# Kernel tuning notes

Measured on AMD Instinct MI355X. Metric: run time of the kernel, lower is better.

## Reference

```python
import jax, jax.numpy as jnp
import numpy as np

N = 50000
C = 128
E = 800000
STEPS = 3


def setup_inputs() -> dict:
    key = jax.random.key(0)
    ks = jax.random.split(key, 8)
    x = jax.random.normal(ks[0], (N, C), dtype=jnp.float32)
    edge_index = jax.random.randint(ks[1], (2, E), 0, N, dtype=jnp.int64)
    s = 1.0 / np.sqrt(C)
    W_lin = jax.random.uniform(ks[2], (C, C), jnp.float32, -s, s)   # nn.Linear(C, C, bias=False)
    W_ih = jax.random.uniform(ks[3], (3 * C, C), jnp.float32, -s, s)  # GRUCell weight_ih
    W_hh = jax.random.uniform(ks[4], (3 * C, C), jnp.float32, -s, s)  # GRUCell weight_hh
    b_ih = jax.random.uniform(ks[5], (3 * C,), jnp.float32, -s, s)
    b_hh = jax.random.uniform(ks[6], (3 * C,), jnp.float32, -s, s)
    return {"x": x, "edge_index": edge_index, "W_lin": W_lin,
            "W_ih": W_ih, "W_hh": W_hh, "b_ih": b_ih, "b_hh": b_hh}


def _gru_cell(inp, h, W_ih, W_hh, b_ih, b_hh):
    # torch.nn.GRUCell math
    gi = inp @ W_ih.T + b_ih   # [N, 3C]
    gh = h @ W_hh.T + b_hh     # [N, 3C]
    i_r, i_z, i_n = jnp.split(gi, 3, axis=-1)
    h_r, h_z, h_n = jnp.split(gh, 3, axis=-1)
    r = jax.nn.sigmoid(i_r + h_r)
    z = jax.nn.sigmoid(i_z + h_z)
    n = jnp.tanh(i_n + r * h_n)
    return (1.0 - z) * n + z * h


def reference(x, edge_index, W_lin, W_ih, W_hh, b_ih, b_hh):
    src = edge_index[0]
    dst = edge_index[1]
    state = x
    for _ in range(STEPS):
        m = state @ W_lin.T                       # [N, C] dense transform
        msgs = jnp.take(m, src, axis=0)           # [E, C] gather
        propagated = jax.ops.segment_sum(msgs, dst, num_segments=N)  # scatter-add
        state = _gru_cell(propagated, state, W_ih, W_hh, b_ih, b_hh)
    return state
```

## Files before the change

### kernel.cpp

```cpp
#include <hip/hip_runtime.h>

#define NN 50000
#define CC 128
#define EE 800000
#define NT 1563
#define NBLK 196

typedef short bf16x8 __attribute__((ext_vector_type(8)));
typedef float f32x4 __attribute__((ext_vector_type(4)));

__device__ __forceinline__ float bf2f(unsigned int u16) {
  union { unsigned int u; float f; } x; x.u = u16 << 16; return x.f;
}
__device__ __forceinline__ unsigned short f2bf(float f) {
  union { float f; unsigned int u; } x; x.f = f;
  unsigned int u = x.u;
  unsigned int r = (u + 0x7fffu + ((u >> 16) & 1u)) >> 16;
  return (unsigned short)r;
}
__device__ __forceinline__ float fsigmoid(float x) {
  return __fdividef(1.f, 1.f + __expf(-x));
}
__device__ __forceinline__ float ftanh(float x) {
  return 1.f - __fdividef(2.f, 1.f + __expf(2.f * x));
}

__global__ void cast_f2b_k(const float* __restrict__ in, unsigned short* __restrict__ out, int n4) {
  int i = blockIdx.x * blockDim.x + threadIdx.x;
  int stride = gridDim.x * blockDim.x;
  for (; i < n4; i += stride) {
    float4 v = ((const float4*)in)[i];
    ushort4 o;
    o.x = f2bf(v.x); o.y = f2bf(v.y); o.z = f2bf(v.z); o.w = f2bf(v.w);
    ((ushort4*)out)[i] = o;
  }
}

__global__ __launch_bounds__(256) void wprep_k(const float* __restrict__ Wih,
                                               const float* __restrict__ Wlin,
                                               const float* __restrict__ Whh,
                                               unsigned short* __restrict__ Wcb,
                                               unsigned short* __restrict__ Whhb) {
  if (blockIdx.x < 192) {
    int gid = blockIdx.x * 256 + threadIdx.x;
    int i = gid >> 7, j = gid & 127;
    float acc = 0.f;
    #pragma unroll 8
    for (int k = 0; k < 128; ++k)
      acc += Wih[i * 128 + k] * Wlin[k * 128 + j];
    Wcb[i * 128 + j] = f2bf(acc);
  } else {
    int i = (blockIdx.x - 192) * 256 + threadIdx.x;
    float4 v = ((const float4*)Whh)[i];
    ushort4 o;
    o.x = f2bf(v.x); o.y = f2bf(v.y); o.z = f2bf(v.z); o.w = f2bf(v.w);
    ((ushort4*)Whhb)[i] = o;
  }
}

__global__ void zero_k(int* __restrict__ p, int n) {
  int i = blockIdx.x * blockDim.x + threadIdx.x;
  if (i < n) p[i] = 0;
}

__global__ void hist_k(const int* __restrict__ dst, int* __restrict__ cntrep,
                       int* __restrict__ rank, int n) {
  int i = blockIdx.x * blockDim.x + threadIdx.x;
  int rep = blockIdx.x & 7;
  if (i < n) rank[i] = atomicAdd(&cntrep[rep * NN + dst[i]], 1);
}

__global__ __launch_bounds__(256) void scan1_k(int* __restrict__ cntrep,
                                               int* __restrict__ rowptr,
                                               int* __restrict__ bsum, int N) {
  __shared__ int wtot[4];
  int tid = threadIdx.x, lane = tid & 63, w = tid >> 6;
  int i = blockIdx.x * 256 + tid;
  int v = 0;
  if (i < N) {
    int s = 0;
    #pragma unroll
    for (int r = 0; r < 8; ++r) {
      int c = cntrep[r * NN + i];
      cntrep[r * NN + i] = s;
      s += c;
    }
    v = s;
  }
  int x = v;
  #pragma unroll
  for (int off = 1; off < 64; off <<= 1) {
    int t = __shfl_up(x, off, 64);
    if (lane >= off) x += t;
  }
  if (lane == 63) wtot[w] = x;
  __syncthreads();
  int woff = 0;
  for (int j = 0; j < w; ++j) woff += wtot[j];
  int excl = x - v + woff;
  if (i < N) rowptr[i] = excl;
  if (tid == 255) bsum[blockIdx.x] = excl + v;
}

__global__ __launch_bounds__(256) void scan2_k(int* __restrict__ bsum, int* __restrict__ rowptr, int NB) {
  __shared__ int wtot[4];
  int tid = threadIdx.x, lane = tid & 63, w = tid >> 6;
  int v = (tid < NB) ? bsum[tid] : 0;
  int x = v;
  #pragma unroll
  for (int off = 1; off < 64; off <<= 1) {
    int t = __shfl_up(x, off, 64);
    if (lane >= off) x += t;
  }
  if (lane == 63) wtot[w] = x;
  __syncthreads();
  int woff = 0;
  for (int j = 0; j < w; ++j) woff += wtot[j];
  int excl = x - v + woff;
  if (tid < NB) bsum[tid] = excl;
  if (tid == 255) rowptr[NN] = excl + v;
}

__global__ void scan3_k(int* __restrict__ rowptr, const int* __restrict__ bsum, int N) {
  int i = blockIdx.x * 256 + threadIdx.x;
  if (i < N) rowptr[i] = rowptr[i] + bsum[i >> 8];
}

__global__ void fill_k(const int* __restrict__ src, const int* __restrict__ dst,
                       const int* __restrict__ rank, const int* __restrict__ rowptr,
                       const int* __restrict__ cntrep, int* __restrict__ colx, int n4) {
  int i = blockIdx.x * blockDim.x + threadIdx.x;
  if (i < n4) {
    int4 s = ((const int4*)src)[i];
    int4 d = ((const int4*)dst)[i];
    int4 r = ((const int4*)rank)[i];
    int base = ((i >> 6) & 7) * NN;
    colx[rowptr[d.x] + cntrep[base + d.x] + r.x] = s.x;
    colx[rowptr[d.y] + cntrep[base + d.y] + r.y] = s.y;
    colx[rowptr[d.z] + cntrep[base + d.z] + r.z] = s.z;
    colx[rowptr[d.w] + cntrep[base + d.w] + r.w] = s.w;
  }
}

__global__ __launch_bounds__(256) void agg3_k(const unsigned short* __restrict__ M,
                                              const int* __restrict__ rowptr,
                                              const int* __restrict__ colx,
                                              unsigned short* __restrict__ P, int N) {
  int wid = (blockIdx.x * 256 + threadIdx.x) >> 6;
  int lane = threadIdx.x & 63;
  if (wid >= N) return;
  int beg = rowptr[wid], end = rowptr[wid + 1];
  int slot = lane >> 4, li = lane & 15;
  float a0 = 0.f, a1 = 0.f, a2 = 0.f, a3 = 0.f, a4 = 0.f, a5 = 0.f, a6 = 0.f, a7 = 0.f;
  #define ACC(v) do { \
    a0 += bf2f((v).x & 0xffffu); a1 += bf2f((v).x >> 16); \
    a2 += bf2f((v).y & 0xffffu); a3 += bf2f((v).y >> 16); \
    a4 += bf2f((v).z & 0xffffu); a5 += bf2f((v).z >> 16); \
    a6 += bf2f((v).w & 0xffffu); a7 += bf2f((v).w >> 16); } while (0)
  int n = end - beg;
  int i = 0;
  for (; i + 16 <= n; i += 16) {
    int e = beg + i + slot;
    int s0 = colx[e], s1 = colx[e + 4], s2 = colx[e + 8], s3 = colx[e + 12];
    uint4 v0 = *(const uint4*)(M + s0 * CC + li * 8);
    uint4 v1 = *(const uint4*)(M + s1 * CC + li * 8);
    uint4 v2 = *(const uint4*)(M + s2 * CC + li * 8);
    uint4 v3 = *(const uint4*)(M + s3 * CC + li * 8);
    ACC(v0); ACC(v1); ACC(v2); ACC(v3);
  }
  for (; i + 4 <= n; i += 4) {
    int e = beg + i + slot;
    int s = colx[e];
    uint4 v = *(const uint4*)(M + s * CC + li * 8);
    ACC(v);
  }
  int rem = n - i;
  if (slot < rem) {
    int e = beg + i + slot;
    int s = colx[e];
    uint4 v = *(const uint4*)(M + s * CC + li * 8);
    ACC(v);
  }
  #undef ACC
  #pragma unroll
  for (int m = 16; m <= 32; m <<= 1) {
    a0 += __shfl_xor(a0, m, 64); a1 += __shfl_xor(a1, m, 64);
    a2 += __shfl_xor(a2, m, 64); a3 += __shfl_xor(a3, m, 64);
    a4 += __shfl_xor(a4, m, 64); a5 += __shfl_xor(a5, m, 64);
    a6 += __shfl_xor(a6, m, 64); a7 += __shfl_xor(a7, m, 64);
  }
  if (slot == 0) {
    uint4 o;
    o.x = (unsigned int)f2bf(a0) | ((unsigned int)f2bf(a1) << 16);
    o.y = (unsigned int)f2bf(a2) | ((unsigned int)f2bf(a3) << 16);
    o.z = (unsigned int)f2bf(a4) | ((unsigned int)f2bf(a5) << 16);
    o.w = (unsigned int)f2bf(a6) | ((unsigned int)f2bf(a7) << 16);
    *(uint4*)(P + wid * CC + li * 8) = o;
  }
}

__global__ __launch_bounds__(512, 2) void gru4_k(const unsigned short* __restrict__ Pb,
                                                 const unsigned short* __restrict__ Sb_in,
                                                 unsigned short* __restrict__ Sb_out,
                                                 float* __restrict__ fout,
                                                 const unsigned short* __restrict__ Wcb,
                                                 const unsigned short* __restrict__ Whhb,
                                                 const float* __restrict__ bih,
                                                 const float* __restrict__ bhh) {
  __shared__ unsigned short sA[2][2][32][128];
  const int tid = threadIdx.x;
  const int lane = tid & 63, w = tid >> 6;
  const int l15 = lane & 15, l4 = lane >> 4;

  const int cg = w * 16 + l15;

  bf16x8 Breg[6][4];
  #pragma unroll
  for (int pi = 0; pi < 6; ++pi) {
    const unsigned short* Wm = (pi < 3) ? Wcb : Whhb;
    int p = (pi < 3) ? pi : pi - 3;
    const unsigned short* base = Wm + (p * 128 + cg) * 128 + l4 * 8;
    #pragma unroll
    for (int ks = 0; ks < 4; ++ks)
      Breg[pi][ks] = *(const bf16x8*)(base + ks * 32);
  }

  const float bir = bih[cg], biz = bih[cg + 128], bin_ = bih[cg + 256];
  const float bhr = bhh[cg], bhz = bhh[cg + 128], bhn = bhh[cg + 256];

  auto loadA = [&](int t, uint4* r) {
    int rowbase = t * 32;
    #pragma unroll
    for (int k = 0; k < 2; ++k) {
      int idx = k * 512 + tid;
      int mat = idx >> 9, j = idx & 511, row = j >> 4, ch = j & 15;
      int grow = rowbase + row;
      const unsigned short* srcp = mat ? Sb_in : Pb;
      r[k] = (grow < NN) ? *(const uint4*)(srcp + grow * 128 + ch * 8) : make_uint4(0, 0, 0, 0);
    }
  };
  auto writeA = [&](int buf, const uint4* r) {
    #pragma unroll
    for (int k = 0; k < 2; ++k) {
      int idx = k * 512 + tid;
      int mat = idx >> 9, j = idx & 511, row = j >> 4, ch = j & 15;
      *(uint4*)&sA[buf][mat][row][((ch ^ (row & 15)) * 8)] = r[k];
    }
  };

  uint4 pre[2];
  int t0 = blockIdx.x;
  loadA(t0, pre);
  writeA(0, pre);
  int cur = 0;
  for (int t = t0; t < NT; t += 256) {
    __syncthreads();
    int tn = t + 256;
    uint4 nxt[2];
    if (tn < NT) loadA(tn, nxt);

    f32x4 acc[6][2] = {};
    #pragma unroll
    for (int ks = 0; ks < 4; ++ks) {
      bf16x8 a[2][2];
      #pragma unroll
      for (int mat = 0; mat < 2; ++mat)
        #pragma unroll
        for (int rt = 0; rt < 2; ++rt) {
          int row = rt * 16 + l15;
          a[mat][rt] = *(const bf16x8*)&sA[cur][mat][row][(((ks * 4 + l4) ^ l15) * 8)];
        }
      #pragma unroll
      for (int pi = 0; pi < 6; ++pi) {
        int am = (pi < 3) ? 0 : 1;
        acc[pi][0] = __builtin_amdgcn_mfma_f32_16x16x32_bf16(a[am][0], Breg[pi][ks], acc[pi][0], 0, 0, 0);
        acc[pi][1] = __builtin_amdgcn_mfma_f32_16x16x32_bf16(a[am][1], Breg[pi][ks], acc[pi][1], 0, 0, 0);
      }
    }

    int rowbase = t * 32;
    #pragma unroll
    for (int rt = 0; rt < 2; ++rt)
      #pragma unroll
      for (int i = 0; i < 4; ++i) {
        int row_loc = rt * 16 + l4 * 4 + i;
        int row = rowbase + row_loc;
        if (row < NN) {
          float gir = acc[0][rt][i] + bir;
          float giz = acc[1][rt][i] + biz;
          float gin = acc[2][rt][i] + bin_;
          float ghr = acc[3][rt][i] + bhr;
          float ghz = acc[4][rt][i] + bhz;
          float ghn = acc[5][rt][i] + bhn;
          float r = fsigmoid(gir + ghr);
          float z = fsigmoid(giz + ghz);
          float n = ftanh(gin + r * ghn);
          float h = bf2f((unsigned int)sA[cur][1][row_loc][(((cg >> 3) ^ (row_loc & 15)) << 3) + (cg & 7)]);
          float o = n + z * (h - n);
          if (fout) fout[row * 128 + cg] = o;
          else      Sb_out[row * 128 + cg] = f2bf(o);
        }
      }
    if (tn < NT) writeA(cur ^ 1, nxt);
    cur ^= 1;
  }
}

extern "C" void kernel_launch(void* const* d_in, const int* in_sizes, int n_in,
                              void* d_out, int out_size, void* d_ws, size_t ws_size,
                              hipStream_t stream) {
  const float* x    = (const float*)d_in[0];
  const int*   ei   = (const int*)d_in[1];
  const float* Wlin = (const float*)d_in[2];
  const float* Wih  = (const float*)d_in[3];
  const float* Whh  = (const float*)d_in[4];
  const float* bih  = (const float*)d_in[5];
  const float* bhh  = (const float*)d_in[6];
  float* out = (float*)d_out;

  char* ws = (char*)d_ws;
  size_t off = 0;
  auto alloc = [&](size_t bytes) -> void* {
    void* p = ws + off;
    off += (bytes + 255) & ~(size_t)255;
    return p;
  };
  unsigned short* SbA  = (unsigned short*)alloc((size_t)NN * CC * 2);
  unsigned short* SbB  = (unsigned short*)alloc((size_t)NN * CC * 2);
  unsigned short* Prb  = (unsigned short*)alloc((size_t)NN * CC * 2);
  unsigned short* Wcb  = (unsigned short*)alloc((size_t)3 * CC * CC * 2);
  unsigned short* Whhb = (unsigned short*)alloc((size_t)3 * CC * CC * 2);
  int* rowptr = (int*)alloc((size_t)(NN + 1) * 4);
  int* cntrep = (int*)alloc((size_t)8 * NN * 4);
  int* rank   = (int*)alloc((size_t)EE * 4);
  int* colx   = (int*)alloc((size_t)EE * 4);
  int* bsum   = (int*)alloc(256 * 4);

  const int* srcI = ei;
  const int* dstI = ei + EE;

  cast_f2b_k<<<1024, 256, 0, stream>>>(x, SbA, NN * CC / 4);
  wprep_k<<<240, 256, 0, stream>>>(Wih, Wlin, Whh, Wcb, Whhb);

  zero_k<<<(8 * NN + 255) / 256, 256, 0, stream>>>(cntrep, 8 * NN);
  hist_k<<<EE / 256, 256, 0, stream>>>(dstI, cntrep, rank, EE);
  scan1_k<<<NBLK, 256, 0, stream>>>(cntrep, rowptr, bsum, NN);
  scan2_k<<<1, 256, 0, stream>>>(bsum, rowptr, NBLK);
  scan3_k<<<NBLK, 256, 0, stream>>>(rowptr, bsum, NN);
  fill_k<<<(EE / 4 + 255) / 256, 256, 0, stream>>>(srcI, dstI, rank, rowptr, cntrep, colx, EE / 4);

  const int aggBlocks = (NN + 3) / 4;

  agg3_k<<<aggBlocks, 256, 0, stream>>>(SbA, rowptr, colx, Prb, NN);
  gru4_k<<<256, 512, 0, stream>>>(Prb, SbA, SbB, nullptr, Wcb, Whhb, bih, bhh);
  agg3_k<<<aggBlocks, 256, 0, stream>>>(SbB, rowptr, colx, Prb, NN);
  gru4_k<<<256, 512, 0, stream>>>(Prb, SbB, SbA, nullptr, Wcb, Whhb, bih, bhh);
  agg3_k<<<aggBlocks, 256, 0, stream>>>(SbA, rowptr, colx, Prb, NN);
  gru4_k<<<256, 512, 0, stream>>>(Prb, SbA, SbB, out, Wcb, Whhb, bih, bhh);
}
```

Baseline: 329.4 us.

## Fuse neighbor aggregation gather into GRU kernel, dropping propagated buffer

Removes the separate aggregation kernel and performs the CSR gather-sum for each 32-row tile inside the GRU kernel's prefetch stage, writing the aggregated row straight into shared memory. This avoids writing and re-reading the propagated bf16 buffer and halves the kernel launches per step. In exchange, each 16-lane group now handles one destination row serially with only 256 persistent blocks, so there is much less memory-level parallelism for the random gathers, and the gather latency sits on the MFMA kernel's critical path.

```diff
diff --git a/kernel.cpp b/kernel.cpp
--- a/kernel.cpp
+++ b/kernel.cpp
@@ -142,67 +142,11 @@
   }
 }
 
-__global__ __launch_bounds__(256) void agg3_k(const unsigned short* __restrict__ M,
-                                              const int* __restrict__ rowptr,
-                                              const int* __restrict__ colx,
-                                              unsigned short* __restrict__ P, int N) {
-  int wid = (blockIdx.x * 256 + threadIdx.x) >> 6;
-  int lane = threadIdx.x & 63;
-  if (wid >= N) return;
-  int beg = rowptr[wid], end = rowptr[wid + 1];
-  int slot = lane >> 4, li = lane & 15;
-  float a0 = 0.f, a1 = 0.f, a2 = 0.f, a3 = 0.f, a4 = 0.f, a5 = 0.f, a6 = 0.f, a7 = 0.f;
-  #define ACC(v) do { \
-    a0 += bf2f((v).x & 0xffffu); a1 += bf2f((v).x >> 16); \
-    a2 += bf2f((v).y & 0xffffu); a3 += bf2f((v).y >> 16); \
-    a4 += bf2f((v).z & 0xffffu); a5 += bf2f((v).z >> 16); \
-    a6 += bf2f((v).w & 0xffffu); a7 += bf2f((v).w >> 16); } while (0)
-  int n = end - beg;
-  int i = 0;
-  for (; i + 16 <= n; i += 16) {
-    int e = beg + i + slot;
-    int s0 = colx[e], s1 = colx[e + 4], s2 = colx[e + 8], s3 = colx[e + 12];
-    uint4 v0 = *(const uint4*)(M + s0 * CC + li * 8);
-    uint4 v1 = *(const uint4*)(M + s1 * CC + li * 8);
-    uint4 v2 = *(const uint4*)(M + s2 * CC + li * 8);
-    uint4 v3 = *(const uint4*)(M + s3 * CC + li * 8);
-    ACC(v0); ACC(v1); ACC(v2); ACC(v3);
-  }
-  for (; i + 4 <= n; i += 4) {
-    int e = beg + i + slot;
-    int s = colx[e];
-    uint4 v = *(const uint4*)(M + s * CC + li * 8);
-    ACC(v);
-  }
-  int rem = n - i;
-  if (slot < rem) {
-    int e = beg + i + slot;
-    int s = colx[e];
-    uint4 v = *(const uint4*)(M + s * CC + li * 8);
-    ACC(v);
-  }
-  #undef ACC
-  #pragma unroll
-  for (int m = 16; m <= 32; m <<= 1) {
-    a0 += __shfl_xor(a0, m, 64); a1 += __shfl_xor(a1, m, 64);
-    a2 += __shfl_xor(a2, m, 64); a3 += __shfl_xor(a3, m, 64);
-    a4 += __shfl_xor(a4, m, 64); a5 += __shfl_xor(a5, m, 64);
-    a6 += __shfl_xor(a6, m, 64); a7 += __shfl_xor(a7, m, 64);
-  }
-  if (slot == 0) {
-    uint4 o;
-    o.x = (unsigned int)f2bf(a0) | ((unsigned int)f2bf(a1) << 16);
-    o.y = (unsigned int)f2bf(a2) | ((unsigned int)f2bf(a3) << 16);
-    o.z = (unsigned int)f2bf(a4) | ((unsigned int)f2bf(a5) << 16);
-    o.w = (unsigned int)f2bf(a6) | ((unsigned int)f2bf(a7) << 16);
-    *(uint4*)(P + wid * CC + li * 8) = o;
-  }
-}
-
-__global__ __launch_bounds__(512, 2) void gru4_k(const unsigned short* __restrict__ Pb,
-                                                 const unsigned short* __restrict__ Sb_in,
+__global__ __launch_bounds__(512, 2) void gru5_k(const unsigned short* __restrict__ Sb_in,
                                                  unsigned short* __restrict__ Sb_out,
                                                  float* __restrict__ fout,
+                                                 const int* __restrict__ rowptr,
+                                                 const int* __restrict__ colx,
                                                  const unsigned short* __restrict__ Wcb,
                                                  const unsigned short* __restrict__ Whhb,
                                                  const float* __restrict__ bih,
@@ -213,6 +157,7 @@
   const int l15 = lane & 15, l4 = lane >> 4;
 
   const int cg = w * 16 + l15;
+  const int growloc = 4 * w + l4;
 
   bf16x8 Breg[6][4];
   #pragma unroll
@@ -228,36 +173,63 @@
   const float bir = bih[cg], biz = bih[cg + 128], bin_ = bih[cg + 256];
   const float bhr = bhh[cg], bhz = bhh[cg + 128], bhn = bhh[cg + 256];
 
-  auto loadA = [&](int t, uint4* r) {
-    int rowbase = t * 32;
-    #pragma unroll
-    for (int k = 0; k < 2; ++k) {
-      int idx = k * 512 + tid;
-      int mat = idx >> 9, j = idx & 511, row = j >> 4, ch = j & 15;
-      int grow = rowbase + row;
-      const unsigned short* srcp = mat ? Sb_in : Pb;
-      r[k] = (grow < NN) ? *(const uint4*)(srcp + grow * 128 + ch * 8) : make_uint4(0, 0, 0, 0);
+  auto loadS = [&](int t, uint4& r) {
+    int row = tid >> 4, ch = tid & 15;
+    int grow = t * 32 + row;
+    r = (grow < NN) ? *(const uint4*)(Sb_in + grow * 128 + ch * 8) : make_uint4(0, 0, 0, 0);
+  };
+  auto writeS = [&](int buf, uint4 r) {
+    int row = tid >> 4, ch = tid & 15;
+    *(uint4*)&sA[buf][1][row][((ch ^ (row & 15)) * 8)] = r;
+  };
+  auto gatherA = [&](int t, uint4& o) {
+    float a0 = 0.f, a1 = 0.f, a2 = 0.f, a3 = 0.f, a4 = 0.f, a5 = 0.f, a6 = 0.f, a7 = 0.f;
+    int grow = t * 32 + growloc;
+    if (grow < NN) {
+      int beg = rowptr[grow], end = rowptr[grow + 1];
+      const unsigned short* Mb = Sb_in + l15 * 8;
+      int e = beg;
+      #define ACC(v) do { \
+        a0 += bf2f((v).x & 0xffffu); a1 += bf2f((v).x >> 16); \
+        a2 += bf2f((v).y & 0xffffu); a3 += bf2f((v).y >> 16); \
+        a4 += bf2f((v).z & 0xffffu); a5 += bf2f((v).z >> 16); \
+        a6 += bf2f((v).w & 0xffffu); a7 += bf2f((v).w >> 16); } while (0)
+      for (; e + 4 <= end; e += 4) {
+        int s0 = colx[e], s1 = colx[e + 1], s2 = colx[e + 2], s3 = colx[e + 3];
+        uint4 v0 = *(const uint4*)(Mb + s0 * 128);
+        uint4 v1 = *(const uint4*)(Mb + s1 * 128);
+        uint4 v2 = *(const uint4*)(Mb + s2 * 128);
+        uint4 v3 = *(const uint4*)(Mb + s3 * 128);
+        ACC(v0); ACC(v1); ACC(v2); ACC(v3);
+      }
+      for (; e < end; ++e) {
+        int s = colx[e];
+        uint4 v = *(const uint4*)(Mb + s * 128);
+        ACC(v);
+      }
+      #undef ACC
     }
-  };
-  auto writeA = [&](int buf, const uint4* r) {
-    #pragma unroll
-    for (int k = 0; k < 2; ++k) {
-      int idx = k * 512 + tid;
-      int mat = idx >> 9, j = idx & 511, row = j >> 4, ch = j & 15;
-      *(uint4*)&sA[buf][mat][row][((ch ^ (row & 15)) * 8)] = r[k];
-    }
-  };
-
-  uint4 pre[2];
+    o.x = (unsigned int)f2bf(a0) | ((unsigned int)f2bf(a1) << 16);
+    o.y = (unsigned int)f2bf(a2) | ((unsigned int)f2bf(a3) << 16);
+    o.z = (unsigned int)f2bf(a4) | ((unsigned int)f2bf(a5) << 16);
+    o.w = (unsigned int)f2bf(a6) | ((unsigned int)f2bf(a7) << 16);
+  };
+  auto writeG = [&](int buf, uint4 o) {
+    *(uint4*)&sA[buf][0][growloc][((l15 ^ (growloc & 15)) * 8)] = o;
+  };
+
   int t0 = blockIdx.x;
-  loadA(t0, pre);
-  writeA(0, pre);
+  uint4 sr, gr;
+  loadS(t0, sr);
+  gatherA(t0, gr);
+  writeS(0, sr);
+  writeG(0, gr);
   int cur = 0;
   for (int t = t0; t < NT; t += 256) {
     __syncthreads();
     int tn = t + 256;
-    uint4 nxt[2];
-    if (tn < NT) loadA(tn, nxt);
+    uint4 sn, gn;
+    if (tn < NT) { loadS(tn, sn); gatherA(tn, gn); }
 
     f32x4 acc[6][2] = {};
     #pragma unroll
@@ -301,7 +273,7 @@
           else      Sb_out[row * 128 + cg] = f2bf(o);
         }
       }
-    if (tn < NT) writeA(cur ^ 1, nxt);
+    if (tn < NT) { writeS(cur ^ 1, sn); writeG(cur ^ 1, gn); }
     cur ^= 1;
   }
 }
@@ -327,7 +299,6 @@
   };
   unsigned short* SbA  = (unsigned short*)alloc((size_t)NN * CC * 2);
   unsigned short* SbB  = (unsigned short*)alloc((size_t)NN * CC * 2);
-  unsigned short* Prb  = (unsigned short*)alloc((size_t)NN * CC * 2);
   unsigned short* Wcb  = (unsigned short*)alloc((size_t)3 * CC * CC * 2);
   unsigned short* Whhb = (unsigned short*)alloc((size_t)3 * CC * CC * 2);
   int* rowptr = (int*)alloc((size_t)(NN + 1) * 4);
@@ -349,12 +320,7 @@
   scan3_k<<<NBLK, 256, 0, stream>>>(rowptr, bsum, NN);
   fill_k<<<(EE / 4 + 255) / 256, 256, 0, stream>>>(srcI, dstI, rank, rowptr, cntrep, colx, EE / 4);
 
-  const int aggBlocks = (NN + 3) / 4;
-
-  agg3_k<<<aggBlocks, 256, 0, stream>>>(SbA, rowptr, colx, Prb, NN);
-  gru4_k<<<256, 512, 0, stream>>>(Prb, SbA, SbB, nullptr, Wcb, Whhb, bih, bhh);
-  agg3_k<<<aggBlocks, 256, 0, stream>>>(SbB, rowptr, colx, Prb, NN);
-  gru4_k<<<256, 512, 0, stream>>>(Prb, SbB, SbA, nullptr, Wcb, Whhb, bih, bhh);
-  agg3_k<<<aggBlocks, 256, 0, stream>>>(SbA, rowptr, colx, Prb, NN);
-  gru4_k<<<256, 512, 0, stream>>>(Prb, SbA, SbB, out, Wcb, Whhb, bih, bhh);
-}
+  gru5_k<<<256, 512, 0, stream>>>(SbA, SbB, nullptr, rowptr, colx, Wcb, Whhb, bih, bhh);
+  gru5_k<<<256, 512, 0, stream>>>(SbB, SbA, nullptr, rowptr, colx, Wcb, Whhb, bih, bhh);
+  gru5_k<<<256, 512, 0, stream>>>(SbA, SbB, out, rowptr, colx, Wcb, Whhb, bih, bhh);
+}
```

Result: slower. 386.6 us (+17.4%).
